# Performance work log

Hardware: AMD Instinct MI355X
Metric: run time of the kernel (lower is better)

## Reference

```python
import jax, jax.numpy as jnp
import numpy as np

B, S, D = 8, 2048, 512

def setup_inputs() -> dict:
    key = jax.random.key(0)
    k1, k2 = jax.random.split(key)
    lstm_out = jax.random.normal(k1, (B, S, D), dtype=jnp.float32)
    # xavier_uniform init for [D, D]
    limit = float(np.sqrt(6.0 / (D + D)))
    attention_weights = jax.random.uniform(k2, (D, D), dtype=jnp.float32, minval=-limit, maxval=limit)
    return {"lstm_out": lstm_out, "attention_weights": attention_weights}

def reference(lstm_out, attention_weights):
    # scores[b,i,j] = tanh( (x W) x^T )
    proj = jnp.einsum('bsd,de->bse', lstm_out, attention_weights)          # [B,S,D]
    scores = jnp.tanh(jnp.einsum('bsd,btd->bst', proj, lstm_out))          # [B,S,S]
    attn = jax.nn.softmax(scores, axis=-1)                                 # [B,S,S]
    return jnp.einsum('bst,btd->bsd', attn, lstm_out)                      # [B,S,D]
```

## Files before the change

kernel.cpp:

```cpp
#include <hip/hip_runtime.h>
#include <hip/hip_bf16.h>

typedef __bf16 bf16;
typedef __attribute__((ext_vector_type(8))) __bf16 bf16x8;
typedef __attribute__((ext_vector_type(4))) __bf16 bf16x4;
typedef __attribute__((ext_vector_type(4))) float floatx4;

__device__ __forceinline__ void gl_lds16(const bf16* g, bf16* l) {
    __builtin_amdgcn_global_load_lds(
        (const __attribute__((address_space(1))) unsigned int*)g,
        (__attribute__((address_space(3))) unsigned int*)l,
        16, 0, 0);
}

__global__ __launch_bounds__(256) void cast_both(const float* __restrict__ in,
                                                 bf16* __restrict__ outn,
                                                 bf16* __restrict__ outt,
                                                 int R, int C) {
    __shared__ float tile[32][33];
    const long long bz = blockIdx.z;
    in   += bz * (long long)R * C;
    outn += bz * (long long)R * C;
    outt += bz * (long long)R * C;
    const int r0 = blockIdx.x * 32, c0 = blockIdx.y * 32;
    const int tx = threadIdx.x & 31, ty = threadIdx.x >> 5;
#pragma unroll
    for (int i = 0; i < 32; i += 8) {
        float v = in[(long long)(r0 + ty + i) * C + (c0 + tx)];
        tile[ty + i][tx] = v;
        outn[(long long)(r0 + ty + i) * C + (c0 + tx)] = (bf16)v;
    }
    __syncthreads();
#pragma unroll
    for (int i = 0; i < 32; i += 8)
        outt[(long long)(c0 + ty + i) * R + (r0 + tx)] = (bf16)tile[tx][ty + i];
}

__global__ __launch_bounds__(256) void cast_transpose(const float* __restrict__ in,
                                                      bf16* __restrict__ out,
                                                      int R, int C) {
    __shared__ float tile[32][33];
    const int r0 = blockIdx.x * 32, c0 = blockIdx.y * 32;
    const int tx = threadIdx.x & 31, ty = threadIdx.x >> 5;
#pragma unroll
    for (int i = 0; i < 32; i += 8)
        tile[ty + i][tx] = in[(long long)(r0 + ty + i) * C + (c0 + tx)];
    __syncthreads();
#pragma unroll
    for (int i = 0; i < 32; i += 8)
        out[(long long)(c0 + ty + i) * R + (r0 + tx)] = (bf16)tile[tx][ty + i];
}

__device__ __forceinline__ float fast_tanh(float v) {
    float e = __expf(2.0f * v);
    return 1.0f - 2.0f / (e + 1.0f);
}

template <int MODE>
__global__ __launch_bounds__(256) void gemm128_nt(const bf16* __restrict__ A,
                                                  const bf16* __restrict__ Bm,
                                                  void* __restrict__ Cout,
                                                  float* __restrict__ rowsum,
                                                  int M, int N, int K,
                                                  long long batchA, long long batchB,
                                                  long long batchC, long long batchR) {
    const long long bz = blockIdx.z;
    A  += bz * batchA;
    Bm += bz * batchB;

    __shared__ bf16 As[128 * 32];
    __shared__ bf16 Bs[128 * 32];
    __shared__ float rs[128];

    const int t    = threadIdx.x;
    const int lane = t & 63;
    const int wave = t >> 6;
    const int quad = lane >> 4;
    const int l16  = lane & 15;

    const int m0 = blockIdx.x * 128;
    const int n0 = blockIdx.y * 128;
    const int wm = (wave >> 1) * 64;
    const int wn = (wave & 1) * 64;

    floatx4 acc[4][4] = {};

    const int r0 = t >> 2;
    const int c0 = (t & 3) * 8;

    const bf16* Ag0 = A + (long long)(m0 + r0) * K + c0;
    const bf16* Ag1 = A + (long long)(m0 + 64 + r0) * K + c0;
    const bf16* Bg0 = Bm + (long long)(n0 + r0) * K + c0;
    const bf16* Bg1 = Bm + (long long)(n0 + 64 + r0) * K + c0;

    for (int k0 = 0; k0 < K; k0 += 32) {
        gl_lds16(Ag0 + k0, &As[t * 8]);
        gl_lds16(Ag1 + k0, &As[(t + 256) * 8]);
        gl_lds16(Bg0 + k0, &Bs[t * 8]);
        gl_lds16(Bg1 + k0, &Bs[(t + 256) * 8]);
        __syncthreads();

        bf16x8 af[4], bfr[4];
#pragma unroll
        for (int i = 0; i < 4; ++i)
            af[i] = *(const bf16x8*)(&As[(wm + i * 16 + l16) * 32 + quad * 8]);
#pragma unroll
        for (int j = 0; j < 4; ++j)
            bfr[j] = *(const bf16x8*)(&Bs[(wn + j * 16 + l16) * 32 + quad * 8]);

#pragma unroll
        for (int i = 0; i < 4; ++i)
#pragma unroll
            for (int j = 0; j < 4; ++j)
                acc[i][j] = __builtin_amdgcn_mfma_f32_16x16x32_bf16(af[i], bfr[j], acc[i][j], 0, 0, 0);

        __syncthreads();
    }

    if (MODE == 0 || MODE == 1) {
        bf16* Cg = (bf16*)Cout + bz * batchC;
        float ps[4][4];
#pragma unroll
        for (int i = 0; i < 4; ++i)
#pragma unroll
            for (int r = 0; r < 4; ++r) ps[i][r] = 0.f;

#pragma unroll
        for (int i = 0; i < 4; ++i)
#pragma unroll
            for (int j = 0; j < 4; ++j)
#pragma unroll
                for (int r = 0; r < 4; ++r) {
                    float v = acc[i][j][r];
                    if (MODE == 1) { v = __expf(fast_tanh(v)); ps[i][r] += v; }
                    long long row = m0 + wm + i * 16 + quad * 4 + r;
                    long long col = n0 + wn + j * 16 + l16;
                    Cg[row * (long long)N + col] = (bf16)v;
                }

        if (MODE == 1) {
#pragma unroll
            for (int i = 0; i < 4; ++i)
#pragma unroll
                for (int r = 0; r < 4; ++r) {
                    float s = ps[i][r];
#pragma unroll
                    for (int msk = 1; msk < 16; msk <<= 1) s += __shfl_xor(s, msk);
                    if (l16 == 0)
                        atomicAdd(&rowsum[bz * batchR + m0 + wm + i * 16 + quad * 4 + r], s);
                }
        }
    } else {
        if (t < 128) rs[t] = rowsum[bz * batchR + m0 + t];
        __syncthreads();
        float* Og = (float*)Cout + bz * batchC;
#pragma unroll
        for (int i = 0; i < 4; ++i)
#pragma unroll
            for (int r = 0; r < 4; ++r) {
                float inv = 1.0f / rs[wm + i * 16 + quad * 4 + r];
                long long row = m0 + wm + i * 16 + quad * 4 + r;
#pragma unroll
                for (int j = 0; j < 4; ++j) {
                    long long col = n0 + wn + j * 16 + l16;
                    Og[row * (long long)N + col] = acc[i][j][r] * inv;
                }
            }
    }
}

extern "C" void kernel_launch(void* const* d_in, const int* in_sizes, int n_in,
                              void* d_out, int out_size, void* d_ws, size_t ws_size,
                              hipStream_t stream) {
    const int B = 8, S = 2048, D = 512;
    const float* x = (const float*)d_in[0];
    const float* W = (const float*)d_in[1];
    float* out = (float*)d_out;

    const size_t nx = (size_t)B * S * D;
    const size_t nw = (size_t)D * D;

    char* ws = (char*)d_ws;
    auto al = [](size_t v) { return (v + 255) & ~(size_t)255; };
    size_t off = 0;
    bf16* xb = (bf16*)(ws + off); off = al(off + nx * 2);
    bf16* xt = (bf16*)(ws + off); off = al(off + nx * 2);
    bf16* pb = (bf16*)(ws + off); off = al(off + nx * 2);
    bf16* wt = (bf16*)(ws + off); off = al(off + nw * 2);
    float* rsum = (float*)(ws + off); off = al(off + (size_t)B * S * 4);
    bf16* sb = (bf16*)(ws + off);
    const size_t full_need = off + (size_t)B * S * S * 2;
    const bool batched = (ws_size >= full_need);

    hipMemsetAsync(rsum, 0, (size_t)B * S * 4, stream);

    { dim3 g(S / 32, D / 32, B); cast_both<<<g, 256, 0, stream>>>(x, xb, xt, S, D); }
    { dim3 g(D / 32, D / 32, 1); cast_transpose<<<g, 256, 0, stream>>>(W, wt, D, D); }

    {
        dim3 g(B * S / 128, D / 128, 1);
        gemm128_nt<0><<<g, 256, 0, stream>>>(xb, wt, (void*)pb, nullptr, B * S, D, D, 0, 0, 0, 0);
    }

    const long long sd = (long long)S * D;
    const long long ss = (long long)S * S;

    if (batched) {
        dim3 g2(S / 128, S / 128, B);
        gemm128_nt<1><<<g2, 256, 0, stream>>>(pb, xb, (void*)sb, rsum, S, S, D, sd, sd, ss, S);
        dim3 g4(S / 128, D / 128, B);
        gemm128_nt<2><<<g4, 256, 0, stream>>>(sb, xt, (void*)out, rsum, S, D, S, ss, sd, sd, S);
    } else {
        for (int b = 0; b < B; ++b) {
            dim3 g2(S / 128, S / 128, 1);
            gemm128_nt<1><<<g2, 256, 0, stream>>>(pb + (size_t)b * sd, xb + (size_t)b * sd,
                                                  (void*)sb, rsum + (size_t)b * S, S, S, D, 0, 0, 0, 0);
            dim3 g4(S / 128, D / 128, 1);
            gemm128_nt<2><<<g4, 256, 0, stream>>>(sb, xt + (size_t)b * sd,
                                                  (void*)(out + (size_t)b * sd), rsum + (size_t)b * S,
                                                  S, D, S, 0, 0, 0, 0);
        }
    }
}
```

Baseline: 233.7 us.

## Use K=64 XOR-swizzled LDS tiles and 64-row tiles for projection and PV GEMMs

Raises the K-step of all GEMMs from 32 to 64 and XOR-swizzles the LDS column layout so fragment reads avoid bank conflicts while halving the number of barrier pairs. The projection and attention-times-V GEMMs move to a 64x128 tile, doubling their block count for better CU occupancy on the small-N problems. The score kernel's epilogue now reduces each row's sum per row directly instead of through a separate partial-sum array. Larger LDS tiles reduce occupancy per CU, and the smaller tiles reload the B operand more often.

```diff
diff --git a/kernel.cpp b/kernel.cpp
--- a/kernel.cpp
+++ b/kernel.cpp
@@ -3,7 +3,6 @@
 
 typedef __bf16 bf16;
 typedef __attribute__((ext_vector_type(8))) __bf16 bf16x8;
-typedef __attribute__((ext_vector_type(4))) __bf16 bf16x4;
 typedef __attribute__((ext_vector_type(4))) float floatx4;
 
 __device__ __forceinline__ void gl_lds16(const bf16* g, bf16* l) {
@@ -56,21 +55,19 @@
     return 1.0f - 2.0f / (e + 1.0f);
 }
 
-template <int MODE>
-__global__ __launch_bounds__(256) void gemm128_nt(const bf16* __restrict__ A,
-                                                  const bf16* __restrict__ Bm,
-                                                  void* __restrict__ Cout,
-                                                  float* __restrict__ rowsum,
-                                                  int M, int N, int K,
-                                                  long long batchA, long long batchB,
-                                                  long long batchC, long long batchR) {
+__global__ __launch_bounds__(256) void gemm128_score(const bf16* __restrict__ A,
+                                                     const bf16* __restrict__ Bm,
+                                                     bf16* __restrict__ P,
+                                                     float* __restrict__ rowsum,
+                                                     int M, int N, int K,
+                                                     long long batchA, long long batchB,
+                                                     long long batchC, long long batchR) {
     const long long bz = blockIdx.z;
     A  += bz * batchA;
     Bm += bz * batchB;
 
-    __shared__ bf16 As[128 * 32];
-    __shared__ bf16 Bs[128 * 32];
-    __shared__ float rs[128];
+    __shared__ bf16 As[128 * 64];
+    __shared__ bf16 Bs[128 * 64];
 
     const int t    = threadIdx.x;
     const int lane = t & 63;
@@ -85,86 +82,152 @@
 
     floatx4 acc[4][4] = {};
 
-    const int r0 = t >> 2;
-    const int c0 = (t & 3) * 8;
-
-    const bf16* Ag0 = A + (long long)(m0 + r0) * K + c0;
-    const bf16* Ag1 = A + (long long)(m0 + 64 + r0) * K + c0;
-    const bf16* Bg0 = Bm + (long long)(n0 + r0) * K + c0;
-    const bf16* Bg1 = Bm + (long long)(n0 + 64 + r0) * K + c0;
-
-    for (int k0 = 0; k0 < K; k0 += 32) {
-        gl_lds16(Ag0 + k0, &As[t * 8]);
-        gl_lds16(Ag1 + k0, &As[(t + 256) * 8]);
-        gl_lds16(Bg0 + k0, &Bs[t * 8]);
-        gl_lds16(Bg1 + k0, &Bs[(t + 256) * 8]);
-        __syncthreads();
-
-        bf16x8 af[4], bfr[4];
+    const int ra = t >> 3;
+    const int ca = (((t & 7) ^ (ra & 7))) * 8;
+    const long long rstep = 32LL * K;
+    const bf16* Abase = A + (long long)(m0 + ra) * K + ca;
+    const bf16* Bbase = Bm + (long long)(n0 + ra) * K + ca;
+
+    const int cq0 = ((quad) ^ (l16 & 7)) * 8;
+    const int cq1 = ((4 + quad) ^ (l16 & 7)) * 8;
+
+    for (int k0 = 0; k0 < K; k0 += 64) {
+#pragma unroll
+        for (int i = 0; i < 4; ++i) {
+            gl_lds16(Abase + k0 + i * rstep, &As[(t + 256 * i) * 8]);
+            gl_lds16(Bbase + k0 + i * rstep, &Bs[(t + 256 * i) * 8]);
+        }
+        __syncthreads();
+
+#pragma unroll
+        for (int s = 0; s < 2; ++s) {
+            const int cq = s ? cq1 : cq0;
+            bf16x8 af[4], bfr[4];
+#pragma unroll
+            for (int i = 0; i < 4; ++i)
+                af[i] = *(const bf16x8*)(&As[(wm + i * 16 + l16) * 64 + cq]);
+#pragma unroll
+            for (int j = 0; j < 4; ++j)
+                bfr[j] = *(const bf16x8*)(&Bs[(wn + j * 16 + l16) * 64 + cq]);
+#pragma unroll
+            for (int i = 0; i < 4; ++i)
+#pragma unroll
+                for (int j = 0; j < 4; ++j)
+                    acc[i][j] = __builtin_amdgcn_mfma_f32_16x16x32_bf16(af[i], bfr[j], acc[i][j], 0, 0, 0);
+        }
+        __syncthreads();
+    }
+
+    bf16* Cg = P + bz * batchC;
+#pragma unroll
+    for (int i = 0; i < 4; ++i)
+#pragma unroll
+        for (int r = 0; r < 4; ++r) {
+            long long row = m0 + wm + i * 16 + quad * 4 + r;
+            float s = 0.f;
+#pragma unroll
+            for (int j = 0; j < 4; ++j) {
+                float v = __expf(fast_tanh(acc[i][j][r]));
+                s += v;
+                Cg[row * (long long)N + (n0 + wn + j * 16 + l16)] = (bf16)v;
+            }
+#pragma unroll
+            for (int msk = 1; msk < 16; msk <<= 1) s += __shfl_xor(s, msk);
+            if (l16 == 0)
+                atomicAdd(&rowsum[bz * batchR + row], s);
+        }
+}
+
+template <int MODE>
+__global__ __launch_bounds__(256) void gemm64_nt(const bf16* __restrict__ A,
+                                                 const bf16* __restrict__ Bm,
+                                                 void* __restrict__ Cout,
+                                                 const float* __restrict__ rowsum,
+                                                 int M, int N, int K,
+                                                 long long batchA, long long batchB,
+                                                 long long batchC, long long batchR) {
+    const long long bz = blockIdx.z;
+    A  += bz * batchA;
+    Bm += bz * batchB;
+
+    __shared__ bf16 As[64 * 64];
+    __shared__ bf16 Bs[128 * 64];
+    __shared__ float rs[64];
+
+    const int t    = threadIdx.x;
+    const int lane = t & 63;
+    const int wave = t >> 6;
+    const int quad = lane >> 4;
+    const int l16  = lane & 15;
+
+    const int m0 = blockIdx.x * 64;
+    const int n0 = blockIdx.y * 128;
+    const int wn = wave * 32;
+
+    floatx4 acc[4][2] = {};
+
+    const int ra = t >> 3;
+    const int ca = (((t & 7) ^ (ra & 7))) * 8;
+    const long long rstep = 32LL * K;
+    const bf16* Abase = A + (long long)(m0 + ra) * K + ca;
+    const bf16* Bbase = Bm + (long long)(n0 + ra) * K + ca;
+
+    const int cq0 = ((quad) ^ (l16 & 7)) * 8;
+    const int cq1 = ((4 + quad) ^ (l16 & 7)) * 8;
+
+    for (int k0 = 0; k0 < K; k0 += 64) {
+#pragma unroll
+        for (int i = 0; i < 2; ++i)
+            gl_lds16(Abase + k0 + i * rstep, &As[(t + 256 * i) * 8]);
 #pragma unroll
         for (int i = 0; i < 4; ++i)
-            af[i] = *(const bf16x8*)(&As[(wm + i * 16 + l16) * 32 + quad * 8]);
-#pragma unroll
-        for (int j = 0; j < 4; ++j)
-            bfr[j] = *(const bf16x8*)(&Bs[(wn + j * 16 + l16) * 32 + quad * 8]);
-
+            gl_lds16(Bbase + k0 + i * rstep, &Bs[(t + 256 * i) * 8]);
+        __syncthreads();
+
+#pragma unroll
+        for (int s = 0; s < 2; ++s) {
+            const int cq = s ? cq1 : cq0;
+            bf16x8 af[4], bfr[2];
+#pragma unroll
+            for (int i = 0; i < 4; ++i)
+                af[i] = *(const bf16x8*)(&As[(i * 16 + l16) * 64 + cq]);
+#pragma unroll
+            for (int j = 0; j < 2; ++j)
+                bfr[j] = *(const bf16x8*)(&Bs[(wn + j * 16 + l16) * 64 + cq]);
+#pragma unroll
+            for (int i = 0; i < 4; ++i)
+#pragma unroll
+                for (int j = 0; j < 2; ++j)
+                    acc[i][j] = __builtin_amdgcn_mfma_f32_16x16x32_bf16(af[i], bfr[j], acc[i][j], 0, 0, 0);
+        }
+        __syncthreads();
+    }
+
+    if (MODE == 2) {
+        if (t < 64) rs[t] = rowsum[bz * batchR + m0 + t];
+        __syncthreads();
+        float* Og = (float*)Cout + bz * batchC;
 #pragma unroll
         for (int i = 0; i < 4; ++i)
 #pragma unroll
-            for (int j = 0; j < 4; ++j)
-                acc[i][j] = __builtin_amdgcn_mfma_f32_16x16x32_bf16(af[i], bfr[j], acc[i][j], 0, 0, 0);
-
-        __syncthreads();
-    }
-
-    if (MODE == 0 || MODE == 1) {
+            for (int r = 0; r < 4; ++r) {
+                int rl = i * 16 + quad * 4 + r;
+                float inv = 1.0f / rs[rl];
+                long long row = m0 + rl;
+#pragma unroll
+                for (int j = 0; j < 2; ++j)
+                    Og[row * (long long)N + (n0 + wn + j * 16 + l16)] = acc[i][j][r] * inv;
+            }
+    } else {
         bf16* Cg = (bf16*)Cout + bz * batchC;
-        float ps[4][4];
 #pragma unroll
         for (int i = 0; i < 4; ++i)
 #pragma unroll
-            for (int r = 0; r < 4; ++r) ps[i][r] = 0.f;
-
-#pragma unroll
-        for (int i = 0; i < 4; ++i)
-#pragma unroll
-            for (int j = 0; j < 4; ++j)
-#pragma unroll
-                for (int r = 0; r < 4; ++r) {
-                    float v = acc[i][j][r];
-                    if (MODE == 1) { v = __expf(fast_tanh(v)); ps[i][r] += v; }
-                    long long row = m0 + wm + i * 16 + quad * 4 + r;
-                    long long col = n0 + wn + j * 16 + l16;
-                    Cg[row * (long long)N + col] = (bf16)v;
-                }
-
-        if (MODE == 1) {
-#pragma unroll
-            for (int i = 0; i < 4; ++i)
-#pragma unroll
-                for (int r = 0; r < 4; ++r) {
-                    float s = ps[i][r];
-#pragma unroll
-                    for (int msk = 1; msk < 16; msk <<= 1) s += __shfl_xor(s, msk);
-                    if (l16 == 0)
-                        atomicAdd(&rowsum[bz * batchR + m0 + wm + i * 16 + quad * 4 + r], s);
-                }
-        }
-    } else {
-        if (t < 128) rs[t] = rowsum[bz * batchR + m0 + t];
-        __syncthreads();
-        float* Og = (float*)Cout + bz * batchC;
-#pragma unroll
-        for (int i = 0; i < 4; ++i)
-#pragma unroll
             for (int r = 0; r < 4; ++r) {
-                float inv = 1.0f / rs[wm + i * 16 + quad * 4 + r];
-                long long row = m0 + wm + i * 16 + quad * 4 + r;
-#pragma unroll
-                for (int j = 0; j < 4; ++j) {
-                    long long col = n0 + wn + j * 16 + l16;
-                    Og[row * (long long)N + col] = acc[i][j][r] * inv;
-                }
+                long long row = m0 + i * 16 + quad * 4 + r;
+#pragma unroll
+                for (int j = 0; j < 2; ++j)
+                    Cg[row * (long long)N + (n0 + wn + j * 16 + l16)] = (bf16)acc[i][j][r];
             }
     }
 }
@@ -198,8 +261,8 @@
     { dim3 g(D / 32, D / 32, 1); cast_transpose<<<g, 256, 0, stream>>>(W, wt, D, D); }
 
     {
-        dim3 g(B * S / 128, D / 128, 1);
-        gemm128_nt<0><<<g, 256, 0, stream>>>(xb, wt, (void*)pb, nullptr, B * S, D, D, 0, 0, 0, 0);
+        dim3 g(B * S / 64, D / 128, 1);
+        gemm64_nt<0><<<g, 256, 0, stream>>>(xb, wt, (void*)pb, nullptr, B * S, D, D, 0, 0, 0, 0);
     }
 
     const long long sd = (long long)S * D;
@@ -207,18 +270,18 @@
 
     if (batched) {
         dim3 g2(S / 128, S / 128, B);
-        gemm128_nt<1><<<g2, 256, 0, stream>>>(pb, xb, (void*)sb, rsum, S, S, D, sd, sd, ss, S);
-        dim3 g4(S / 128, D / 128, B);
-        gemm128_nt<2><<<g4, 256, 0, stream>>>(sb, xt, (void*)out, rsum, S, D, S, ss, sd, sd, S);
+        gemm128_score<<<g2, 256, 0, stream>>>(pb, xb, sb, rsum, S, S, D, sd, sd, ss, S);
+        dim3 g4(S / 64, D / 128, B);
+        gemm64_nt<2><<<g4, 256, 0, stream>>>(sb, xt, (void*)out, rsum, S, D, S, ss, sd, sd, S);
     } else {
         for (int b = 0; b < B; ++b) {
             dim3 g2(S / 128, S / 128, 1);
-            gemm128_nt<1><<<g2, 256, 0, stream>>>(pb + (size_t)b * sd, xb + (size_t)b * sd,
-                                                  (void*)sb, rsum + (size_t)b * S, S, S, D, 0, 0, 0, 0);
-            dim3 g4(S / 128, D / 128, 1);
-            gemm128_nt<2><<<g4, 256, 0, stream>>>(sb, xt + (size_t)b * sd,
-                                                  (void*)(out + (size_t)b * sd), rsum + (size_t)b * S,
-                                                  S, D, S, 0, 0, 0, 0);
-        }
-    }
-}
+            gemm128_score<<<g2, 256, 0, stream>>>(pb + (size_t)b * sd, xb + (size_t)b * sd,
+                                                  sb, rsum + (size_t)b * S, S, S, D, 0, 0, 0, 0);
+            dim3 g4(S / 64, D / 128, 1);
+            gemm64_nt<2><<<g4, 256, 0, stream>>>(sb, xt + (size_t)b * sd,
+                                                 (void*)(out + (size_t)b * sd), rsum + (size_t)b * S,
+                                                 S, D, S, 0, 0, 0, 0);
+        }
+    }
+}
```

Measured after the change: 215.7 us. 7.7% less time.

## Enlarge GEMM tiles to 256x128x64 with XOR-swizzled LDS layout

Applied to the files above, without the earlier changes.

Replaces the 128x128x32 GEMM tile with a 256x128 tile and K-step 64, so each wave computes a 128x64 sub-tile (8x4 MFMA accumulators). LDS rows are XOR-swizzled by row index to avoid bank conflicts on the wider 64-element rows. The goal is more MFMA work per global load and per barrier. In exchange it doubles the accumulator registers and LDS use (48KB), which lowers occupancy, and halves the block count; the score GEMM grid drops to 1024 blocks and the output GEMM to 256.

```diff
diff --git a/kernel.cpp b/kernel.cpp
--- a/kernel.cpp
+++ b/kernel.cpp
@@ -3,7 +3,6 @@
 
 typedef __bf16 bf16;
 typedef __attribute__((ext_vector_type(8))) __bf16 bf16x8;
-typedef __attribute__((ext_vector_type(4))) __bf16 bf16x4;
 typedef __attribute__((ext_vector_type(4))) float floatx4;
 
 __device__ __forceinline__ void gl_lds16(const bf16* g, bf16* l) {
@@ -57,20 +56,20 @@
 }
 
 template <int MODE>
-__global__ __launch_bounds__(256) void gemm128_nt(const bf16* __restrict__ A,
-                                                  const bf16* __restrict__ Bm,
-                                                  void* __restrict__ Cout,
-                                                  float* __restrict__ rowsum,
-                                                  int M, int N, int K,
-                                                  long long batchA, long long batchB,
-                                                  long long batchC, long long batchR) {
+__global__ __launch_bounds__(256) void gemm256(const bf16* __restrict__ A,
+                                               const bf16* __restrict__ Bm,
+                                               void* __restrict__ Cout,
+                                               float* __restrict__ rowsum,
+                                               int M, int N, int K,
+                                               long long batchA, long long batchB,
+                                               long long batchC, long long batchR) {
     const long long bz = blockIdx.z;
     A  += bz * batchA;
     Bm += bz * batchB;
 
-    __shared__ bf16 As[128 * 32];
-    __shared__ bf16 Bs[128 * 32];
-    __shared__ float rs[128];
+    __shared__ bf16 As[256 * 64];
+    __shared__ bf16 Bs[128 * 64];
+    __shared__ float rs[256];
 
     const int t    = threadIdx.x;
     const int lane = t & 63;
@@ -78,92 +77,83 @@
     const int quad = lane >> 4;
     const int l16  = lane & 15;
 
-    const int m0 = blockIdx.x * 128;
+    const int m0 = blockIdx.x * 256;
     const int n0 = blockIdx.y * 128;
-    const int wm = (wave >> 1) * 64;
+    const int wm = (wave >> 1) * 128;
     const int wn = (wave & 1) * 64;
 
-    floatx4 acc[4][4] = {};
-
-    const int r0 = t >> 2;
-    const int c0 = (t & 3) * 8;
-
-    const bf16* Ag0 = A + (long long)(m0 + r0) * K + c0;
-    const bf16* Ag1 = A + (long long)(m0 + 64 + r0) * K + c0;
-    const bf16* Bg0 = Bm + (long long)(n0 + r0) * K + c0;
-    const bf16* Bg1 = Bm + (long long)(n0 + 64 + r0) * K + c0;
-
-    for (int k0 = 0; k0 < K; k0 += 32) {
-        gl_lds16(Ag0 + k0, &As[t * 8]);
-        gl_lds16(Ag1 + k0, &As[(t + 256) * 8]);
-        gl_lds16(Bg0 + k0, &Bs[t * 8]);
-        gl_lds16(Bg1 + k0, &Bs[(t + 256) * 8]);
+    floatx4 acc[8][4] = {};
+
+    const int ra = t >> 3;
+    const int ca = (((t & 7) ^ (ra & 7))) * 8;
+    const long long rstep = 32LL * K;
+    const bf16* Abase = A + (long long)(m0 + ra) * K + ca;
+    const bf16* Bbase = Bm + (long long)(n0 + ra) * K + ca;
+
+    const int cq0 = ((quad) ^ (l16 & 7)) * 8;
+    const int cq1 = ((4 + quad) ^ (l16 & 7)) * 8;
+
+    for (int k0 = 0; k0 < K; k0 += 64) {
+#pragma unroll
+        for (int i = 0; i < 8; ++i)
+            gl_lds16(Abase + k0 + i * rstep, &As[(t + 256 * i) * 8]);
+#pragma unroll
+        for (int i = 0; i < 4; ++i)
+            gl_lds16(Bbase + k0 + i * rstep, &Bs[(t + 256 * i) * 8]);
         __syncthreads();
 
-        bf16x8 af[4], bfr[4];
-#pragma unroll
-        for (int i = 0; i < 4; ++i)
-            af[i] = *(const bf16x8*)(&As[(wm + i * 16 + l16) * 32 + quad * 8]);
-#pragma unroll
-        for (int j = 0; j < 4; ++j)
-            bfr[j] = *(const bf16x8*)(&Bs[(wn + j * 16 + l16) * 32 + quad * 8]);
-
-#pragma unroll
-        for (int i = 0; i < 4; ++i)
+#pragma unroll
+        for (int s = 0; s < 2; ++s) {
+            const int cq = s ? cq1 : cq0;
+            bf16x8 af[8], bfr[4];
+#pragma unroll
+            for (int i = 0; i < 8; ++i)
+                af[i] = *(const bf16x8*)(&As[(wm + i * 16 + l16) * 64 + cq]);
 #pragma unroll
             for (int j = 0; j < 4; ++j)
-                acc[i][j] = __builtin_amdgcn_mfma_f32_16x16x32_bf16(af[i], bfr[j], acc[i][j], 0, 0, 0);
-
+                bfr[j] = *(const bf16x8*)(&Bs[(wn + j * 16 + l16) * 64 + cq]);
+#pragma unroll
+            for (int i = 0; i < 8; ++i)
+#pragma unroll
+                for (int j = 0; j < 4; ++j)
+                    acc[i][j] = __builtin_amdgcn_mfma_f32_16x16x32_bf16(af[i], bfr[j], acc[i][j], 0, 0, 0);
+        }
         __syncthreads();
     }
 
-    if (MODE == 0 || MODE == 1) {
-        bf16* Cg = (bf16*)Cout + bz * batchC;
-        float ps[4][4];
-#pragma unroll
-        for (int i = 0; i < 4; ++i)
-#pragma unroll
-            for (int r = 0; r < 4; ++r) ps[i][r] = 0.f;
-
-#pragma unroll
-        for (int i = 0; i < 4; ++i)
-#pragma unroll
-            for (int j = 0; j < 4; ++j)
-#pragma unroll
-                for (int r = 0; r < 4; ++r) {
-                    float v = acc[i][j][r];
-                    if (MODE == 1) { v = __expf(fast_tanh(v)); ps[i][r] += v; }
-                    long long row = m0 + wm + i * 16 + quad * 4 + r;
-                    long long col = n0 + wn + j * 16 + l16;
-                    Cg[row * (long long)N + col] = (bf16)v;
-                }
-
-        if (MODE == 1) {
-#pragma unroll
-            for (int i = 0; i < 4; ++i)
-#pragma unroll
-                for (int r = 0; r < 4; ++r) {
-                    float s = ps[i][r];
-#pragma unroll
-                    for (int msk = 1; msk < 16; msk <<= 1) s += __shfl_xor(s, msk);
-                    if (l16 == 0)
-                        atomicAdd(&rowsum[bz * batchR + m0 + wm + i * 16 + quad * 4 + r], s);
-                }
-        }
-    } else {
-        if (t < 128) rs[t] = rowsum[bz * batchR + m0 + t];
+    if (MODE == 2) {
+        rs[t] = rowsum[bz * batchR + m0 + t];
         __syncthreads();
         float* Og = (float*)Cout + bz * batchC;
 #pragma unroll
-        for (int i = 0; i < 4; ++i)
+        for (int i = 0; i < 8; ++i)
 #pragma unroll
             for (int r = 0; r < 4; ++r) {
-                float inv = 1.0f / rs[wm + i * 16 + quad * 4 + r];
+                int rl = wm + i * 16 + quad * 4 + r;
+                float inv = 1.0f / rs[rl];
+                long long row = m0 + rl;
+#pragma unroll
+                for (int j = 0; j < 4; ++j)
+                    Og[row * (long long)N + (n0 + wn + j * 16 + l16)] = acc[i][j][r] * inv;
+            }
+    } else {
+        bf16* Cg = (bf16*)Cout + bz * batchC;
+#pragma unroll
+        for (int i = 0; i < 8; ++i)
+#pragma unroll
+            for (int r = 0; r < 4; ++r) {
                 long long row = m0 + wm + i * 16 + quad * 4 + r;
+                float sum = 0.f;
 #pragma unroll
                 for (int j = 0; j < 4; ++j) {
-                    long long col = n0 + wn + j * 16 + l16;
-                    Og[row * (long long)N + col] = acc[i][j][r] * inv;
+                    float v = acc[i][j][r];
+                    if (MODE == 1) { v = __expf(fast_tanh(v)); sum += v; }
+                    Cg[row * (long long)N + (n0 + wn + j * 16 + l16)] = (bf16)v;
+                }
+                if (MODE == 1) {
+#pragma unroll
+                    for (int msk = 1; msk < 16; msk <<= 1) sum += __shfl_xor(sum, msk);
+                    if (l16 == 0) atomicAdd(&rowsum[bz * batchR + row], sum);
                 }
             }
     }
@@ -198,27 +188,27 @@
     { dim3 g(D / 32, D / 32, 1); cast_transpose<<<g, 256, 0, stream>>>(W, wt, D, D); }
 
     {
-        dim3 g(B * S / 128, D / 128, 1);
-        gemm128_nt<0><<<g, 256, 0, stream>>>(xb, wt, (void*)pb, nullptr, B * S, D, D, 0, 0, 0, 0);
+        dim3 g(B * S / 256, D / 128, 1);
+        gemm256<0><<<g, 256, 0, stream>>>(xb, wt, (void*)pb, nullptr, B * S, D, D, 0, 0, 0, 0);
     }
 
     const long long sd = (long long)S * D;
     const long long ss = (long long)S * S;
 
     if (batched) {
-        dim3 g2(S / 128, S / 128, B);
-        gemm128_nt<1><<<g2, 256, 0, stream>>>(pb, xb, (void*)sb, rsum, S, S, D, sd, sd, ss, S);
-        dim3 g4(S / 128, D / 128, B);
-        gemm128_nt<2><<<g4, 256, 0, stream>>>(sb, xt, (void*)out, rsum, S, D, S, ss, sd, sd, S);
+        dim3 g2(S / 256, S / 128, B);
+        gemm256<1><<<g2, 256, 0, stream>>>(pb, xb, (void*)sb, rsum, S, S, D, sd, sd, ss, S);
+        dim3 g4(S / 256, D / 128, B);
+        gemm256<2><<<g4, 256, 0, stream>>>(sb, xt, (void*)out, rsum, S, D, S, ss, sd, sd, S);
     } else {
         for (int b = 0; b < B; ++b) {
-            dim3 g2(S / 128, S / 128, 1);
-            gemm128_nt<1><<<g2, 256, 0, stream>>>(pb + (size_t)b * sd, xb + (size_t)b * sd,
-                                                  (void*)sb, rsum + (size_t)b * S, S, S, D, 0, 0, 0, 0);
-            dim3 g4(S / 128, D / 128, 1);
-            gemm128_nt<2><<<g4, 256, 0, stream>>>(sb, xt + (size_t)b * sd,
-                                                  (void*)(out + (size_t)b * sd), rsum + (size_t)b * S,
-                                                  S, D, S, 0, 0, 0, 0);
+            dim3 g2(S / 256, S / 128, 1);
+            gemm256<1><<<g2, 256, 0, stream>>>(pb + (size_t)b * sd, xb + (size_t)b * sd,
+                                               (void*)sb, rsum + (size_t)b * S, S, S, D, 0, 0, 0, 0);
+            dim3 g4(S / 256, D / 128, 1);
+            gemm256<2><<<g4, 256, 0, stream>>>(sb, xt + (size_t)b * sd,
+                                               (void*)(out + (size_t)b * sd), rsum + (size_t)b * S,
+                                               S, D, S, 0, 0, 0, 0);
         }
     }
 }
```

After: 266.1 us. +13.8%, slower.
